# Kernel optimization log

Measured on AMD Instinct MI355X. Metric: run time of the kernel, lower is better.

Reference implementation:

```python
import jax, jax.numpy as jnp
import numpy as np

HOPS = 4
ALPHA = 0.1
N = 100000   # nodes
E = 1600000  # edges (before self loops)
DX = 128     # x feature dim
DY = 32      # y (soft label) dim


def setup_inputs() -> dict:
    key = jax.random.key(0)
    k1, k2, k3, k4 = jax.random.split(key, 4)
    x = jax.random.normal(k1, (N, DX), dtype=jnp.float32)
    y = jax.random.normal(k2, (N, DY), dtype=jnp.float32)
    src = jax.random.randint(k3, (E,), 0, N)
    dst = jax.random.randint(k4, (E,), 0, N)
    # emulate remove_self_loops with static shapes: perturb any accidental self loop
    dst = jnp.where(src == dst, (dst + 1) % N, dst)
    edge_index = jnp.stack([src, dst]).astype(jnp.int64)
    return {"x": x, "y": y, "edge_index": edge_index}


def reference(x, y, edge_index):
    src, dst = edge_index[0], edge_index[1]
    # add_self_loops (edge_index already has self loops removed)
    loop = jnp.arange(N, dtype=src.dtype)
    src = jnp.concatenate([src, loop])
    dst = jnp.concatenate([dst, loop])
    # symmetric normalization: w_e = deg(src)^-1/2 * deg(dst)^-1/2, deg counted on dst
    deg = jax.ops.segment_sum(jnp.ones_like(dst, dtype=x.dtype), dst, num_segments=N)
    dinv = jnp.where(deg > 0, deg ** -0.5, 0.0)
    w = dinv[src] * dinv[dst]  # [E+N]

    def spmm(v):
        # adj[src, dst] = w  =>  (adj @ v)[i] = sum_{e: src_e = i} w_e * v[dst_e]
        return jax.ops.segment_sum(w[:, None] * v[dst], src, num_segments=N)

    for _ in range(HOPS):
        x_prime = spmm(x)
        y_prime = spmm(y)
        if ALPHA > 0:
            x_prime = (1.0 - ALPHA) * x_prime + ALPHA * x
            y_prime = (1.0 - ALPHA) * y_prime + ALPHA * y
        x, y = x_prime, y_prime
    return x, y
```

## Files before the change

kernel.cpp:

```cpp
#include <hip/hip_runtime.h>
#include <hip/hip_fp16.h>


#define NN 100000
#define EE 1600000
#define NPAD 100096
#define NBKT 391
#define CHUNK 4096
#define CAP3 1280
#define EMAX 5120

#define GETREG_XCC_IMM (((32 - 1) << 11) | (0 << 6) | 20)

__device__ __forceinline__ unsigned packh(float a, float b) {
    __half2 h = __floats2half2_rn(a, b);
    return *reinterpret_cast<unsigned*>(&h);
}
__device__ __forceinline__ void acc8(float* a, uint4 w, float m) {
    const __half2* h = reinterpret_cast<const __half2*>(&w);
    #pragma unroll
    for (int i = 0; i < 4; ++i) {
        a[2 * i]     = fmaf(m, __half2float(__low2half(h[i])),  a[2 * i]);
        a[2 * i + 1] = fmaf(m, __half2float(__high2half(h[i])), a[2 * i + 1]);
    }
}
__device__ __forceinline__ void unp8(float* c, uint4 w) {
    const __half2* h = reinterpret_cast<const __half2*>(&w);
    #pragma unroll
    for (int i = 0; i < 4; ++i) {
        float2 f = __half22float2(h[i]);
        c[2 * i] = f.x; c[2 * i + 1] = f.y;
    }
}


__global__ void zero_kernel(int* __restrict__ bufs, int total,
                            const int* __restrict__ raw, int* __restrict__ flag) {
    int i = blockIdx.x * blockDim.x + threadIdx.x;
    if (i < total) bufs[i] = 0;
    if (i == 0) {
        int is64 = 1;
        for (int k = 1; k < 16; k += 2) {
            if (raw[k] != 0) { is64 = 0; break; }
        }
        *flag = is64;
    }
}

__global__ __launch_bounds__(512) void passA_kernel(const void* __restrict__ raw,
                                                    const int* __restrict__ flag,
                                                    int* __restrict__ indeg_rep,
                                                    int* __restrict__ gbcur,
                                                    int* __restrict__ buf) {
    __shared__ unsigned short sh_b[CHUNK];
    __shared__ unsigned int   sh_p[CHUNK];
    __shared__ unsigned int   sh_sorted[CHUNK];
    __shared__ unsigned short sh_bs[CHUNK];
    __shared__ int hist[512];
    __shared__ int excl[512];
    __shared__ int gbase[512];
    __shared__ int lcur[512];

    int tid = threadIdx.x;
    int base = blockIdx.x * CHUNK;
    int nval = EE - base; if (nval > CHUNK) nval = CHUNK;
    int r = __builtin_amdgcn_s_getreg(GETREG_XCC_IMM) & 7;
    int is64 = *flag;

    hist[tid] = 0;
    __syncthreads();

    for (int i = tid; i < nval; i += 512) {
        int e = base + i;
        int s, d;
        if (is64) {
            s = (int)((const long long*)raw)[e];
            d = (int)((const long long*)raw)[EE + e];
        } else {
            s = ((const int*)raw)[e];
            d = ((const int*)raw)[EE + e];
        }
        atomicAdd(&indeg_rep[r * NPAD + d], 1);
        int b = s >> 8;
        sh_b[i] = (unsigned short)b;
        sh_p[i] = ((unsigned)(s & 255) << 17) | (unsigned)d;
        atomicAdd(&hist[b], 1);
    }
    __syncthreads();

    excl[tid] = hist[tid];
    __syncthreads();
    for (int off = 1; off < 512; off <<= 1) {
        int t = (tid >= off) ? excl[tid - off] : 0;
        __syncthreads();
        excl[tid] += t;
        __syncthreads();
    }
    int inc = excl[tid];
    int h = hist[tid];
    int e = inc - h;
    excl[tid] = e;
    lcur[tid] = e;
    if (h > 0) gbase[tid] = atomicAdd(&gbcur[(tid * 8 + r) * 16], h);
    __syncthreads();

    for (int i = tid; i < nval; i += 512) {
        int b = sh_b[i];
        int pos = atomicAdd(&lcur[b], 1);
        sh_sorted[pos] = sh_p[i];
        sh_bs[pos] = (unsigned short)b;
    }
    __syncthreads();

    for (int i = tid; i < nval; i += 512) {
        int b = sh_bs[i];
        int gpos = gbase[b] + (i - excl[b]);
        if (gpos < CAP3)
            buf[((size_t)b * 8 + r) * CAP3 + gpos] = (int)sh_sorted[i];
    }
}

__global__ void bucket_scan_kernel(const int* __restrict__ gbcur, int* __restrict__ bucket_base,
                                   int* __restrict__ rowptr) {
    __shared__ int s[512];
    int tid = threadIdx.x;
    int v = 0;
    if (tid < NBKT) {
        int run = 0;
        #pragma unroll
        for (int r = 0; r < 8; ++r) {
            int c = gbcur[(tid * 8 + r) * 16];
            c = (c < CAP3) ? c : CAP3;
            run = (run + c < EMAX) ? run + c : EMAX;
        }
        v = run;
    }
    s[tid] = v;
    __syncthreads();
    for (int off = 1; off < 512; off <<= 1) {
        int t = (tid >= off) ? s[tid - off] : 0;
        __syncthreads();
        s[tid] += t;
        __syncthreads();
    }
    if (tid < NBKT) bucket_base[tid] = s[tid] - v;
    if (tid == 0) rowptr[NN] = EE;
}

__global__ void dinv_kernel(const int* __restrict__ indeg_rep, float* __restrict__ dinv) {
    int i = blockIdx.x * blockDim.x + threadIdx.x;
    if (i < NN) {
        int ind = 1;
        #pragma unroll
        for (int r = 0; r < 8; ++r) ind += indeg_rep[r * NPAD + i];
        dinv[i] = rsqrtf((float)ind);
    }
}

__global__ void cast_kernel(const float4* __restrict__ x0, const float4* __restrict__ y0,
                            const float* __restrict__ dinv, uint4* __restrict__ zx,
                            uint4* __restrict__ zy) {
    int t = blockIdx.x * blockDim.x + threadIdx.x;
    if (t < NN * 16) {
        int node = t >> 4, c = t & 15;
        float di = dinv[node];
        float4 a = x0[(size_t)node * 32 + c * 2];
        float4 b = x0[(size_t)node * 32 + c * 2 + 1];
        uint4 o;
        o.x = packh(di * a.x, di * a.y); o.y = packh(di * a.z, di * a.w);
        o.z = packh(di * b.x, di * b.y); o.w = packh(di * b.z, di * b.w);
        zx[(size_t)node * 16 + c] = o;
    } else if (t < NN * 20) {
        int u = t - NN * 16;
        int node = u >> 2, c = u & 3;
        float di = dinv[node];
        float4 a = y0[(size_t)node * 8 + c * 2];
        float4 b = y0[(size_t)node * 8 + c * 2 + 1];
        uint4 o;
        o.x = packh(di * a.x, di * a.y); o.y = packh(di * a.z, di * a.w);
        o.z = packh(di * b.x, di * b.y); o.w = packh(di * b.z, di * b.w);
        zy[(size_t)node * 4 + c] = o;
    }
}

__global__ __launch_bounds__(256) void passB_kernel(const int* __restrict__ gbcur,
                                                    const int* __restrict__ buf,
                                                    const int* __restrict__ bucket_base,
                                                    int* __restrict__ rowptr,
                                                    int* __restrict__ dst_sorted) {
    int b = blockIdx.x;
    int tid = threadIdx.x;
    __shared__ int cnt[8], off[9];
    __shared__ int edges[EMAX];
    __shared__ int hist[256];
    __shared__ int sc[256];
    __shared__ int base_s;

    if (tid < 8) {
        int c = gbcur[(b * 8 + tid) * 16];
        cnt[tid] = (c < CAP3) ? c : CAP3;
    }
    hist[tid] = 0;
    __syncthreads();
    if (tid == 0) {
        int run = 0;
        #pragma unroll
        for (int r = 0; r < 8; ++r) {
            off[r] = run;
            run = (run + cnt[r] < EMAX) ? run + cnt[r] : EMAX;
        }
        off[8] = run;
        base_s = bucket_base[b];
    }
    __syncthreads();
    #pragma unroll
    for (int r = 0; r < 8; ++r) {
        int c = off[r + 1] - off[r];
        const int* src = buf + ((size_t)b * 8 + r) * CAP3;
        for (int i = tid; i < c; i += 256) edges[off[r] + i] = src[i];
    }
    __syncthreads();
    int total = off[8];
    for (int i = tid; i < total; i += 256) atomicAdd(&hist[edges[i] >> 17], 1);
    __syncthreads();
    int hv = hist[tid];
    sc[tid] = hv;
    __syncthreads();
    for (int o = 1; o < 256; o <<= 1) {
        int t = (tid >= o) ? sc[tid - o] : 0;
        __syncthreads();
        sc[tid] += t;
        __syncthreads();
    }
    int excl = sc[tid] - hv;
    int node = (b << 8) + tid;
    if (node < NN) rowptr[node] = base_s + excl;
    hist[tid] = excl;
    __syncthreads();
    for (int i = tid; i < total; i += 256) {
        int p = edges[i];
        int pos = atomicAdd(&hist[p >> 17], 1);
        dst_sorted[base_s + pos] = p & 0x1ffff;
    }
}

template <bool OUTH>
__global__ __launch_bounds__(256) void hop_kernel(const int* __restrict__ rowptr,
                                                  const int* __restrict__ dst_sorted,
                                                  const float* __restrict__ dinv,
                                                  const uint4* __restrict__ zx,
                                                  const uint4* __restrict__ zy,
                                                  void* __restrict__ nx,
                                                  void* __restrict__ ny) {
    int t = blockIdx.x * blockDim.x + threadIdx.x;
    int row = t >> 6, lane = t & 63;
    if (row >= NN) return;
    int beg = rowptr[row], end = rowptr[row + 1];
    float di = dinv[row];

    int g = lane >> 4, sub = lane & 15;
    int gy = lane >> 2, sy = lane & 3;

    float ax[8] = {0.f, 0.f, 0.f, 0.f, 0.f, 0.f, 0.f, 0.f};
    float ay[8] = {0.f, 0.f, 0.f, 0.f, 0.f, 0.f, 0.f, 0.f};

    int last = (end > beg) ? end - 1 : beg;
    for (int e0 = beg; e0 < end; e0 += 16) {
        int ex0 = e0 + g, ex1 = e0 + 4 + g, ex2 = e0 + 8 + g, ex3 = e0 + 12 + g;
        int ey = e0 + gy;
        int d0 = dst_sorted[min(ex0, last)];
        int d1 = dst_sorted[min(ex1, last)];
        int d2 = dst_sorted[min(ex2, last)];
        int d3 = dst_sorted[min(ex3, last)];
        int dy = dst_sorted[min(ey, last)];
        uint4 w0 = zx[(size_t)d0 * 16 + sub];
        uint4 w1 = zx[(size_t)d1 * 16 + sub];
        uint4 w2 = zx[(size_t)d2 * 16 + sub];
        uint4 w3 = zx[(size_t)d3 * 16 + sub];
        uint4 wy = zy[(size_t)dy * 4 + sy];
        float m0 = (ex0 <= last) ? 1.f : 0.f;
        float m1 = (ex1 <= last) ? 1.f : 0.f;
        float m2 = (ex2 <= last) ? 1.f : 0.f;
        float m3 = (ex3 <= last) ? 1.f : 0.f;
        float my = (ey  <= last) ? 1.f : 0.f;

        acc8(ax, w0, m0);
        acc8(ax, w1, m1);
        acc8(ax, w2, m2);
        acc8(ax, w3, m3);
        acc8(ay, wy, my);
    }

    #pragma unroll
    for (int m = 16; m <= 32; m <<= 1) {
        #pragma unroll
        for (int i = 0; i < 8; ++i) ax[i] += __shfl_xor(ax[i], m);
    }
    #pragma unroll
    for (int m = 4; m <= 32; m <<= 1) {
        #pragma unroll
        for (int i = 0; i < 8; ++i) ay[i] += __shfl_xor(ay[i], m);
    }

    float sg = 0.9f * di;
    float sl = 0.9f * di + 0.1f / di;

    if (g == 0) {
        uint4 wz = zx[(size_t)row * 16 + sub];
        float c[8];
        unp8(c, wz);
        float r[8];
        #pragma unroll
        for (int i = 0; i < 8; ++i) r[i] = sg * ax[i] + sl * c[i];
        if constexpr (OUTH) {
            uint4 o;
            o.x = packh(di * r[0], di * r[1]); o.y = packh(di * r[2], di * r[3]);
            o.z = packh(di * r[4], di * r[5]); o.w = packh(di * r[6], di * r[7]);
            ((uint4*)nx)[(size_t)row * 16 + sub] = o;
        } else {
            float4 a, b;
            a.x = r[0]; a.y = r[1]; a.z = r[2]; a.w = r[3];
            b.x = r[4]; b.y = r[5]; b.z = r[6]; b.w = r[7];
            ((float4*)nx)[(size_t)row * 32 + sub * 2]     = a;
            ((float4*)nx)[(size_t)row * 32 + sub * 2 + 1] = b;
        }
    }
    if (gy == 0) {
        uint4 wz = zy[(size_t)row * 4 + sy];
        float c[8];
        unp8(c, wz);
        float r[8];
        #pragma unroll
        for (int i = 0; i < 8; ++i) r[i] = sg * ay[i] + sl * c[i];
        if constexpr (OUTH) {
            uint4 o;
            o.x = packh(di * r[0], di * r[1]); o.y = packh(di * r[2], di * r[3]);
            o.z = packh(di * r[4], di * r[5]); o.w = packh(di * r[6], di * r[7]);
            ((uint4*)ny)[(size_t)row * 4 + sy] = o;
        } else {
            float4 a, b;
            a.x = r[0]; a.y = r[1]; a.z = r[2]; a.w = r[3];
            b.x = r[4]; b.y = r[5]; b.z = r[6]; b.w = r[7];
            ((float4*)ny)[(size_t)row * 8 + sy * 2]     = a;
            ((float4*)ny)[(size_t)row * 8 + sy * 2 + 1] = b;
        }
    }
}

extern "C" void kernel_launch(void* const* d_in, const int* in_sizes, int n_in,
                              void* d_out, int out_size, void* d_ws, size_t ws_size,
                              hipStream_t stream) {
    const float* x0  = (const float*)d_in[0];
    const float* y0  = (const float*)d_in[1];
    const void*  raw = d_in[2];

    float* out_x = (float*)d_out;
    float* out_y = out_x + (size_t)NN * 128;

    int*   flag        = (int*)d_ws;
    int*   indeg_rep   = flag + 16;
    int*   gbcur       = indeg_rep + 8 * NPAD;
    int*   bucket_base = gbcur + 512 * 8 * 16;
    int*   rowptr      = bucket_base + 512;
    float* dinv        = (float*)(rowptr + 100112);
    int*   dst_sorted  = (int*)(dinv + NPAD);
    uint4* zxA         = (uint4*)(dst_sorted + EE);
    uint4* zxB         = zxA + (size_t)NN * 16;
    uint4* zyA         = (uint4*)(zxB + (size_t)NN * 16);
    int*   buf         = (int*)(zyA + (size_t)NN * 4);
    uint4* zyB         = (uint4*)buf;

    const int B = 256;
    const int GW = (NN * 64 + B - 1) / B;
    const int ZTOT = 8 * NPAD + 512 * 8 * 16;

    zero_kernel<<<(ZTOT + B - 1) / B, B, 0, stream>>>(indeg_rep, ZTOT, (const int*)raw, flag);
    passA_kernel<<<(EE + CHUNK - 1) / CHUNK, 512, 0, stream>>>(raw, flag, indeg_rep, gbcur, buf);
    bucket_scan_kernel<<<1, 512, 0, stream>>>(gbcur, bucket_base, rowptr);
    dinv_kernel<<<(NN + B - 1) / B, B, 0, stream>>>(indeg_rep, dinv);
    cast_kernel<<<(NN * 20 + B - 1) / B, B, 0, stream>>>(
        (const float4*)x0, (const float4*)y0, dinv, zxA, zyA);
    passB_kernel<<<NBKT, 256, 0, stream>>>(gbcur, buf, bucket_base, rowptr, dst_sorted);

    hop_kernel<true><<<GW, B, 0, stream>>>(rowptr, dst_sorted, dinv, zxA, zyA, zxB, zyB);
    hop_kernel<true><<<GW, B, 0, stream>>>(rowptr, dst_sorted, dinv, zxB, zyB, zxA, zyA);
    hop_kernel<true><<<GW, B, 0, stream>>>(rowptr, dst_sorted, dinv, zxA, zyA, zxB, zyB);
    hop_kernel<false><<<GW, B, 0, stream>>>(rowptr, dst_sorted, dinv, zxB, zyB, out_x, out_y);
}
```

Baseline: 586.4 us.

## Compute in-degree via bucketed dst binning instead of global atomics

Replaces the per-edge global atomicAdd on replicated in-degree arrays with a second in-block bucket sort by destination high bits in passA, writing low bytes into per-bucket/per-XCC buffers. A new passB2 kernel then histograms each bucket in shared memory to produce in-degrees. This removes scattered global atomics and the zeroing of 8 replicated degree arrays, at the cost of an extra in-block sort pass, extra byte buffer traffic and an extra kernel launch.

Result: faster. 545.5 us (-7.0%).

```diff
diff --git a/kernel.cpp b/kernel.cpp
--- a/kernel.cpp
+++ b/kernel.cpp
@@ -49,9 +49,10 @@
 
 __global__ __launch_bounds__(512) void passA_kernel(const void* __restrict__ raw,
                                                     const int* __restrict__ flag,
-                                                    int* __restrict__ indeg_rep,
                                                     int* __restrict__ gbcur,
-                                                    int* __restrict__ buf) {
+                                                    int* __restrict__ gdcur,
+                                                    int* __restrict__ buf,
+                                                    unsigned char* __restrict__ dbuf) {
     __shared__ unsigned short sh_b[CHUNK];
     __shared__ unsigned int   sh_p[CHUNK];
     __shared__ unsigned int   sh_sorted[CHUNK];
@@ -80,7 +81,6 @@
             s = ((const int*)raw)[e];
             d = ((const int*)raw)[EE + e];
         }
-        atomicAdd(&indeg_rep[r * NPAD + d], 1);
         int b = s >> 8;
         sh_b[i] = (unsigned short)b;
         sh_p[i] = ((unsigned)(s & 255) << 17) | (unsigned)d;
@@ -96,12 +96,14 @@
         excl[tid] += t;
         __syncthreads();
     }
-    int inc = excl[tid];
-    int h = hist[tid];
-    int e = inc - h;
-    excl[tid] = e;
-    lcur[tid] = e;
-    if (h > 0) gbase[tid] = atomicAdd(&gbcur[(tid * 8 + r) * 16], h);
+    {
+        int inc = excl[tid];
+        int h = hist[tid];
+        int e = inc - h;
+        excl[tid] = e;
+        lcur[tid] = e;
+        if (h > 0) gbase[tid] = atomicAdd(&gbcur[(tid * 8 + r) * 16], h);
+    }
     __syncthreads();
 
     for (int i = tid; i < nval; i += 512) {
@@ -117,6 +119,50 @@
         int gpos = gbase[b] + (i - excl[b]);
         if (gpos < CAP3)
             buf[((size_t)b * 8 + r) * CAP3 + gpos] = (int)sh_sorted[i];
+    }
+    __syncthreads();
+
+    hist[tid] = 0;
+    __syncthreads();
+    for (int i = tid; i < nval; i += 512) {
+        int d = (int)(sh_p[i] & 0x1ffffu);
+        int db = d >> 8;
+        sh_b[i] = (unsigned short)db;
+        atomicAdd(&hist[db], 1);
+    }
+    __syncthreads();
+
+    excl[tid] = hist[tid];
+    __syncthreads();
+    for (int off = 1; off < 512; off <<= 1) {
+        int t = (tid >= off) ? excl[tid - off] : 0;
+        __syncthreads();
+        excl[tid] += t;
+        __syncthreads();
+    }
+    {
+        int inc = excl[tid];
+        int h = hist[tid];
+        int e = inc - h;
+        excl[tid] = e;
+        lcur[tid] = e;
+        if (h > 0) gbase[tid] = atomicAdd(&gdcur[(tid * 8 + r) * 16], h);
+    }
+    __syncthreads();
+
+    for (int i = tid; i < nval; i += 512) {
+        int db = sh_b[i];
+        int pos = atomicAdd(&lcur[db], 1);
+        sh_sorted[pos] = sh_p[i] & 255u;
+        sh_bs[pos] = (unsigned short)db;
+    }
+    __syncthreads();
+
+    for (int i = tid; i < nval; i += 512) {
+        int db = sh_bs[i];
+        int gpos = gbase[db] + (i - excl[db]);
+        if (gpos < CAP3)
+            dbuf[((size_t)db * 8 + r) * CAP3 + gpos] = (unsigned char)sh_sorted[i];
     }
 }
 
@@ -147,12 +193,34 @@
     if (tid == 0) rowptr[NN] = EE;
 }
 
-__global__ void dinv_kernel(const int* __restrict__ indeg_rep, float* __restrict__ dinv) {
+__global__ __launch_bounds__(256) void passB2_kernel(const int* __restrict__ gdcur,
+                                                     const unsigned char* __restrict__ dbuf,
+                                                     int* __restrict__ indeg) {
+    int b = blockIdx.x;
+    int tid = threadIdx.x;
+    __shared__ int hist[256];
+    __shared__ int cnt[8];
+    hist[tid] = 0;
+    if (tid < 8) {
+        int c = gdcur[(b * 8 + tid) * 16];
+        cnt[tid] = (c < CAP3) ? c : CAP3;
+    }
+    __syncthreads();
+    #pragma unroll
+    for (int r = 0; r < 8; ++r) {
+        int c = cnt[r];
+        const unsigned char* src = dbuf + ((size_t)b * 8 + r) * CAP3;
+        for (int i = tid; i < c; i += 256) atomicAdd(&hist[src[i]], 1);
+    }
+    __syncthreads();
+    int node = (b << 8) + tid;
+    if (node < NN) indeg[node] = hist[tid];
+}
+
+__global__ void dinv_kernel(const int* __restrict__ indeg, float* __restrict__ dinv) {
     int i = blockIdx.x * blockDim.x + threadIdx.x;
     if (i < NN) {
-        int ind = 1;
-        #pragma unroll
-        for (int r = 0; r < 8; ++r) ind += indeg_rep[r * NPAD + i];
+        int ind = 1 + indeg[i];
         dinv[i] = rsqrtf((float)ind);
     }
 }
@@ -358,26 +426,29 @@
     float* out_y = out_x + (size_t)NN * 128;
 
     int*   flag        = (int*)d_ws;
-    int*   indeg_rep   = flag + 16;
-    int*   gbcur       = indeg_rep + 8 * NPAD;
-    int*   bucket_base = gbcur + 512 * 8 * 16;
+    int*   gbcur       = flag + 16;
+    int*   gdcur       = gbcur + 512 * 8 * 16;
+    int*   bucket_base = gdcur + 512 * 8 * 16;
     int*   rowptr      = bucket_base + 512;
-    float* dinv        = (float*)(rowptr + 100112);
+    int*   indeg       = rowptr + 100112;
+    float* dinv        = (float*)(indeg + NPAD);
     int*   dst_sorted  = (int*)(dinv + NPAD);
     uint4* zxA         = (uint4*)(dst_sorted + EE);
     uint4* zxB         = zxA + (size_t)NN * 16;
     uint4* zyA         = (uint4*)(zxB + (size_t)NN * 16);
     int*   buf         = (int*)(zyA + (size_t)NN * 4);
+    unsigned char* dbuf = (unsigned char*)(buf + (size_t)NBKT * 8 * CAP3);
     uint4* zyB         = (uint4*)buf;
 
     const int B = 256;
     const int GW = (NN * 64 + B - 1) / B;
-    const int ZTOT = 8 * NPAD + 512 * 8 * 16;
-
-    zero_kernel<<<(ZTOT + B - 1) / B, B, 0, stream>>>(indeg_rep, ZTOT, (const int*)raw, flag);
-    passA_kernel<<<(EE + CHUNK - 1) / CHUNK, 512, 0, stream>>>(raw, flag, indeg_rep, gbcur, buf);
+    const int ZTOT = 2 * 512 * 8 * 16;
+
+    zero_kernel<<<(ZTOT + B - 1) / B, B, 0, stream>>>(gbcur, ZTOT, (const int*)raw, flag);
+    passA_kernel<<<(EE + CHUNK - 1) / CHUNK, 512, 0, stream>>>(raw, flag, gbcur, gdcur, buf, dbuf);
     bucket_scan_kernel<<<1, 512, 0, stream>>>(gbcur, bucket_base, rowptr);
-    dinv_kernel<<<(NN + B - 1) / B, B, 0, stream>>>(indeg_rep, dinv);
+    passB2_kernel<<<NBKT, 256, 0, stream>>>(gdcur, dbuf, indeg);
+    dinv_kernel<<<(NN + B - 1) / B, B, 0, stream>>>(indeg, dinv);
     cast_kernel<<<(NN * 20 + B - 1) / B, B, 0, stream>>>(
         (const float4*)x0, (const float4*)y0, dinv, zxA, zyA);
     passB_kernel<<<NBKT, 256, 0, stream>>>(gbcur, buf, bucket_base, rowptr, dst_sorted);
```
